# Optimization experiments

Measured on AMD Instinct MI355X. Metric: run time of the kernel, lower is better.

## Reference

```python
import jax, jax.numpy as jnp
import numpy as np

T = 4096          # tokens (batch*seq)
DIM = 2048        # model dim
INTER = 1024      # moe_inter_dim
E = 32            # n_routed_experts
TOPK = 6          # n_activated_experts
G = 8             # n_expert_groups
TOPK_G = 4        # n_limited_groups
SHARED_INTER = 2 * INTER  # n_shared_experts * moe_inter_dim
ROUTE_SCALE = 1.0


def setup_inputs() -> dict:
    key = jax.random.key(0)
    ks = jax.random.split(key, 8)
    s = 0.02
    return {
        "x": jax.random.normal(ks[0], (T, DIM), jnp.float32),
        "gate_w": jax.random.normal(ks[1], (E, DIM), jnp.float32) * s,
        "wg": jax.random.normal(ks[2], (E, DIM, INTER), jnp.float32) * s,   # gate_proj (stored [in,out])
        "wu": jax.random.normal(ks[3], (E, DIM, INTER), jnp.float32) * s,   # up_proj
        "wd": jax.random.normal(ks[4], (E, INTER, DIM), jnp.float32) * s,   # down_proj
        "swg": jax.random.normal(ks[5], (DIM, SHARED_INTER), jnp.float32) * s,
        "swu": jax.random.normal(ks[6], (DIM, SHARED_INTER), jnp.float32) * s,
        "swd": jax.random.normal(ks[7], (SHARED_INTER, DIM), jnp.float32) * s,
    }


def _gate(x, gate_w):
    # scores = softmax(x @ W^T); bias is None since dim != 7168 -> group score = amax
    scores = jax.nn.softmax(x @ gate_w.T, axis=-1)          # [T, E]
    orig = scores
    gs = scores.reshape(x.shape[0], G, E // G)              # [T, G, E/G]
    group_scores = gs.max(axis=-1)                          # [T, G]
    _, gidx = jax.lax.top_k(group_scores, TOPK_G)           # [T, TOPK_G]
    gmask = jnp.zeros((x.shape[0], G), bool).at[
        jnp.arange(x.shape[0])[:, None], gidx].set(True)
    masked = jnp.where(gmask[:, :, None], gs, -jnp.inf).reshape(x.shape[0], E)
    _, idx = jax.lax.top_k(masked, TOPK)                    # [T, TOPK]
    w = jnp.take_along_axis(orig, idx, axis=1) * ROUTE_SCALE  # softmax path: no renorm
    return w, idx


def reference(x, gate_w, wg, wu, wd, swg, swu, swd):
    weights, indices = _gate(x, gate_w)
    # combine[t, e] = routing weight of expert e for token t (0 if not selected)
    combine = (jax.nn.one_hot(indices, E, dtype=x.dtype) * weights[..., None]).sum(axis=1)  # [T, E]
    y = jnp.zeros_like(x)
    for e in range(E):  # fixed small loop over structurally distinct expert params
        h = jax.nn.silu(x @ wg[e]) * (x @ wu[e])            # [T, INTER]
        y = y + (h @ wd[e]) * combine[:, e:e + 1]
    shared = (jax.nn.silu(x @ swg) * (x @ swu)) @ swd       # shared experts MLP
    return y + shared
```

## Files before the change

### kernel.cpp

```cpp
#include <hip/hip_runtime.h>
#include <hip/hip_bf16.h>

typedef float f32x4 __attribute__((ext_vector_type(4)));
typedef __bf16 bf16x8 __attribute__((ext_vector_type(8)));
typedef unsigned short u16;

#define T_TOK 4096
#define DIMK 2048
#define INTERN 1024
#define NEXP 32
#define NTOPK 6
#define NGRP 8
#define NTOPG 4
#define SINTER 2048
#define MAXPADROWS 29184

__device__ __forceinline__ void glds16(const void* g, void* l) {
    auto* gp = (const __attribute__((address_space(1))) int*)(g);
    auto* lp = (__attribute__((address_space(3))) int*)(l);
    __builtin_amdgcn_global_load_lds(gp, lp, 16, 0, 0);
}

__device__ __forceinline__ size_t toff(int row, int k, int K) {
    int g = (k >> 3) & 7;
    return (size_t)(row >> 7) * (size_t)(128 * K) + (size_t)(k >> 6) * 8192 +
           (size_t)((row & 127) * 64 + ((g ^ (row & 7)) << 3) + (k & 7));
}

template <bool CAT>
__device__ __forceinline__ void tile_trans_512(const float* __restrict__ src, int JD, int k0, int j0,
                                               u16* __restrict__ ob, int KOUT, int s, float* tile) {
    const int tid = threadIdx.x;
    {
        const int r = tid >> 3, c8 = (tid & 7) * 8;
        float4 v0 = *reinterpret_cast<const float4*>(&src[(size_t)(k0 + r) * JD + j0 + c8]);
        float4 v1 = *reinterpret_cast<const float4*>(&src[(size_t)(k0 + r) * JD + j0 + c8 + 4]);
        float* tp = &tile[r * 65 + c8];
        tp[0] = v0.x; tp[1] = v0.y; tp[2] = v0.z; tp[3] = v0.w;
        tp[4] = v1.x; tp[5] = v1.y; tp[6] = v1.z; tp[7] = v1.w;
    }
    __syncthreads();
    {
        const int jl = tid >> 3, kh = (tid & 7) * 8;
        const int j = j0 + jl;
        const int n = CAT ? (((j >> 4) << 5) + s * 16 + (j & 15)) : j;
        bf16x8 o;
#pragma unroll
        for (int jj = 0; jj < 8; ++jj) o[jj] = (__bf16)tile[(kh + jj) * 65 + jl];
        *reinterpret_cast<bf16x8*>(ob + toff(n, k0 + kh, KOUT)) = o;
    }
}

__device__ __forceinline__ void gate_wave(const float* __restrict__ x, const float* __restrict__ gw, int t,
                                          int* __restrict__ counts, int* __restrict__ ids,
                                          int* __restrict__ tok2row, float* __restrict__ wtok,
                                          float* __restrict__ logits) {
    const int lane = threadIdx.x & 63;
    const float4* xr = reinterpret_cast<const float4*>(x + (size_t)t * DIMK);
    for (int e = 0; e < NEXP; ++e) {
        const float4* gr = reinterpret_cast<const float4*>(gw + (size_t)e * DIMK);
        float acc = 0.f;
#pragma unroll
        for (int i = 0; i < DIMK / 4 / 64; ++i) {
            float4 xv = xr[lane + i * 64];
            float4 gv = gr[lane + i * 64];
            acc += xv.x * gv.x + xv.y * gv.y + xv.z * gv.z + xv.w * gv.w;
        }
#pragma unroll
        for (int s = 32; s; s >>= 1) acc += __shfl_xor(acc, s);
        if (lane == 0) logits[e] = acc;
    }
    if (lane != 0) return;
    float sc[NEXP];
#pragma unroll
    for (int e = 0; e < NEXP; ++e) sc[e] = logits[e];
    float mx = sc[0];
#pragma unroll
    for (int e = 1; e < NEXP; ++e) mx = fmaxf(mx, sc[e]);
    float ssum = 0.f;
#pragma unroll
    for (int e = 0; e < NEXP; ++e) { sc[e] = __expf(sc[e] - mx); ssum += sc[e]; }
    const float inv = 1.f / ssum;
    float gsc[NGRP];
#pragma unroll
    for (int g = 0; g < NGRP; ++g) {
        float m2 = sc[g * 4];
#pragma unroll
        for (int j = 1; j < 4; ++j) m2 = fmaxf(m2, sc[g * 4 + j]);
        gsc[g] = m2;
    }
    int gsel = 0;
    for (int r = 0; r < NTOPG; ++r) {
        float bv = -1.f; int bi = 0;
#pragma unroll
        for (int g = 0; g < NGRP; ++g) {
            bool c = (((gsel >> g) & 1) == 0) && (gsc[g] > bv);
            bv = c ? gsc[g] : bv; bi = c ? g : bi;
        }
        gsel |= (1 << bi);
    }
    float msk[NEXP];
#pragma unroll
    for (int e = 0; e < NEXP; ++e) msk[e] = ((gsel >> (e >> 2)) & 1) ? sc[e] : -1.f;
    for (int r = 0; r < NTOPK; ++r) {
        float bv = -3.f; int bi = 0;
#pragma unroll
        for (int e = 0; e < NEXP; ++e) {
            bool c = msk[e] > bv;
            bv = c ? msk[e] : bv; bi = c ? e : bi;
        }
#pragma unroll
        for (int e = 0; e < NEXP; ++e) if (e == bi) msk[e] = -2.f;
        float w = bv * inv;
        int slot = atomicAdd(&counts[bi], 1);
        ids[bi * T_TOK + slot] = t;
        tok2row[t * NTOPK + r] = (bi << 12) | slot;
        wtok[t * NTOPK + r] = w;
    }
}

__global__ __launch_bounds__(512) void prep_kernel(
    const float* __restrict__ x, const float* __restrict__ gate_w,
    const float* __restrict__ swg, const float* __restrict__ swu, const float* __restrict__ swd,
    const float* __restrict__ wg, const float* __restrict__ wu,
    u16* __restrict__ xbT, u16* __restrict__ WcatS, u16* __restrict__ swdT, u16* __restrict__ WcatE,
    int* __restrict__ counts, int* __restrict__ ids, int* __restrict__ tok2row, float* __restrict__ wtok) {
    __shared__ float tile[64 * 65];
    int lin = blockIdx.x;
    if (lin < 512) {
        int w = threadIdx.x >> 6;
        gate_wave(x, gate_w, lin * 8 + w, counts, ids, tok2row, wtok, &tile[w * 33]);
    } else if (lin < 2560) {
        int gi = ((lin - 512) * 512 + threadIdx.x) * 8;
        int row = gi >> 11, k = gi & 2047;
        const float4* p = reinterpret_cast<const float4*>(x + gi);
        float4 a = p[0], b = p[1];
        bf16x8 v;
        v[0] = (__bf16)a.x; v[1] = (__bf16)a.y; v[2] = (__bf16)a.z; v[3] = (__bf16)a.w;
        v[4] = (__bf16)b.x; v[5] = (__bf16)b.y; v[6] = (__bf16)b.z; v[7] = (__bf16)b.w;
        *reinterpret_cast<bf16x8*>(xbT + toff(row, k, DIMK)) = v;
    } else if (lin < 4608) {
        int v = lin - 2560;
        int s = v >> 10, u = v & 1023;
        int kt = (u >> 5) & 31, jt = u & 31;
        tile_trans_512<true>((s ? swu : swg), SINTER, kt * 64, jt * 64, WcatS, DIMK, s, tile);
    } else if (lin < 5632) {
        int v = lin - 4608;
        int kt = v >> 5, jt = v & 31;
        tile_trans_512<false>(swd, DIMK, kt * 64, jt * 64, swdT, SINTER, 0, tile);
    } else {
        int u = lin - 5632;
        int e = u >> 10, v = u & 1023;
        int s = (v >> 9) & 1, kt = (v >> 4) & 31, jt = v & 15;
        const float* src = (s ? wu : wg) + (size_t)e * DIMK * INTERN;
        u16* ob = WcatE + (size_t)e * 2048 * DIMK;
        tile_trans_512<true>(src, INTERN, kt * 64, jt * 64, ob, DIMK, s, tile);
    }
}

__global__ void scan_kernel(const int* __restrict__ counts, int* __restrict__ poff) {
    if (threadIdx.x == 0) {
        int o = 0;
        for (int e = 0; e < NEXP; ++e) { poff[e] = o; o += (counts[e] + 127) & ~127; }
    }
}

__device__ __forceinline__ void dev_gemm1(u16* smem, const u16* __restrict__ xbT, const u16* __restrict__ b0,
                                          u16* __restrict__ ho, int bm, int bn, int M, int Mpad, int hbase,
                                          int HKdim, bool gath, int e, const int* __restrict__ ids) {
    u16* Alds = smem;
    u16* Blds = smem + 32768;
    constexpr int NT = DIMK / 64;
    const int tid = threadIdx.x;
    const int t8 = tid * 8;
    size_t aSrc[2][2];
#pragma unroll
    for (int h = 0; h < 2; ++h)
#pragma unroll
        for (int j = 0; j < 2; ++j) {
            int drow = j * 64 + (tid >> 3);
            int row = bm * 256 + h * 128 + drow;
            int tok;
            if (gath) { int cr = row < M ? row : M - 1; tok = ids[e * T_TOK + cr]; }
            else tok = row;
            int slot = (tid & 7) ^ (drow & 7) ^ (tok & 7);
            aSrc[h][j] = (size_t)(tok >> 7) * (size_t)(128 * 2048) + (size_t)((tok & 127) * 64 + slot * 8);
        }
    const u16* bCh[2] = { b0 + (size_t)(2 * bn + 0) * (128 * 2048), b0 + (size_t)(2 * bn + 1) * (128 * 2048) };

    const int lane = tid & 63, wv = tid >> 6;
    const int wr = wv >> 2, wc = wv & 3;
    const int l15 = lane & 15, lk = lane >> 4;

    f32x4 acc[8][4];
#pragma unroll
    for (int m = 0; m < 8; ++m)
#pragma unroll
        for (int n = 0; n < 4; ++n) acc[m][n] = {0.f, 0.f, 0.f, 0.f};

    auto SA = [&](int kt, int h, int buf) {
        glds16(xbT + aSrc[h][0] + (size_t)kt * 8192, &Alds[buf * 16384 + h * 8192 + t8]);
        glds16(xbT + aSrc[h][1] + (size_t)kt * 8192, &Alds[buf * 16384 + h * 8192 + 4096 + t8]);
    };
    auto SB = [&](int kt, int h, int buf) {
        glds16(bCh[h] + (size_t)kt * 8192 + t8, &Blds[buf * 16384 + h * 8192 + t8]);
        glds16(bCh[h] + (size_t)kt * 8192 + 4096 + t8, &Blds[buf * 16384 + h * 8192 + 4096 + t8]);
    };
    bf16x8 afr[4][2], bfr0[2][2], bfr1[2][2];
    auto DSRA = [&](int buf, int mh) {
#pragma unroll
        for (int mi = 0; mi < 4; ++mi)
#pragma unroll
            for (int ki = 0; ki < 2; ++ki) {
                int rl = wr * 128 + mh * 64 + mi * 16 + l15;
                int g = ki * 4 + lk;
                afr[mi][ki] = *reinterpret_cast<const bf16x8*>(
                    &Alds[buf * 16384 + (rl >> 7) * 8192 + (rl & 127) * 64 + ((g ^ (rl & 7)) << 3)]);
            }
    };
    auto DSRB = [&](int buf, int nh, bf16x8 (&bf)[2][2]) {
#pragma unroll
        for (int nj = 0; nj < 2; ++nj)
#pragma unroll
            for (int ki = 0; ki < 2; ++ki) {
                int rc = wc * 64 + (nh * 2 + nj) * 16 + l15;
                int g = ki * 4 + lk;
                bf[nj][ki] = *reinterpret_cast<const bf16x8*>(
                    &Blds[buf * 16384 + (rc >> 7) * 8192 + (rc & 127) * 64 + ((g ^ (rc & 7)) << 3)]);
            }
    };

    SA(0, 0, 0); SA(0, 1, 0);
    SB(0, 0, 0); SB(0, 1, 0);
    SB(1, 0, 1); SB(1, 1, 1);
    asm volatile("s_waitcnt vmcnt(4)" ::: "memory");
    __builtin_amdgcn_s_barrier();

#pragma unroll 1
    for (int t = 0; t < NT; ++t) {
        const int abuf = t & 1;
        const int bbuf = t % 3;
        const int b3 = (t + 2) % 3;
        DSRA(abuf, 0);
        DSRB(bbuf, 0, bfr0);
        if (t + 1 < NT) { SA(t + 1, 0, abuf ^ 1); SA(t + 1, 1, abuf ^ 1); }
        __builtin_amdgcn_s_barrier();
        __builtin_amdgcn_s_setprio(1);
#pragma unroll
        for (int ki = 0; ki < 2; ++ki)
#pragma unroll
            for (int mi = 0; mi < 4; ++mi)
#pragma unroll
                for (int nj = 0; nj < 2; ++nj)
                    acc[mi][nj] = __builtin_amdgcn_mfma_f32_16x16x32_bf16(afr[mi][ki], bfr0[nj][ki], acc[mi][nj], 0, 0, 0);
        __builtin_amdgcn_s_setprio(0);
        __builtin_amdgcn_s_barrier();
        DSRB(bbuf, 1, bfr1);
        if (t + 2 < NT) SB(t + 2, 0, b3);
        __builtin_amdgcn_s_barrier();
        __builtin_amdgcn_s_setprio(1);
#pragma unroll
        for (int ki = 0; ki < 2; ++ki)
#pragma unroll
            for (int mi = 0; mi < 4; ++mi)
#pragma unroll
                for (int nj = 0; nj < 2; ++nj)
                    acc[mi][2 + nj] = __builtin_amdgcn_mfma_f32_16x16x32_bf16(afr[mi][ki], bfr1[nj][ki], acc[mi][2 + nj], 0, 0, 0);
        __builtin_amdgcn_s_setprio(0);
        __builtin_amdgcn_s_barrier();
        DSRA(abuf, 1);
        if (t + 2 < NT) SB(t + 2, 1, b3);
        __builtin_amdgcn_s_barrier();
        __builtin_amdgcn_s_setprio(1);
#pragma unroll
        for (int ki = 0; ki < 2; ++ki)
#pragma unroll
            for (int mi = 0; mi < 4; ++mi)
#pragma unroll
                for (int nj = 0; nj < 2; ++nj)
                    acc[4 + mi][2 + nj] = __builtin_amdgcn_mfma_f32_16x16x32_bf16(afr[mi][ki], bfr1[nj][ki], acc[4 + mi][2 + nj], 0, 0, 0);
        __builtin_amdgcn_s_setprio(0);
        __builtin_amdgcn_s_barrier();
        __builtin_amdgcn_s_setprio(1);
#pragma unroll
        for (int ki = 0; ki < 2; ++ki)
#pragma unroll
            for (int mi = 0; mi < 4; ++mi)
#pragma unroll
                for (int nj = 0; nj < 2; ++nj)
                    acc[4 + mi][nj] = __builtin_amdgcn_mfma_f32_16x16x32_bf16(afr[mi][ki], bfr0[nj][ki], acc[4 + mi][nj], 0, 0, 0);
        __builtin_amdgcn_s_setprio(0);
        if (t + 2 < NT) { asm volatile("s_waitcnt vmcnt(4)" ::: "memory"); }
        else { asm volatile("s_waitcnt vmcnt(0)" ::: "memory"); }
        __builtin_amdgcn_s_barrier();
    }

#pragma unroll
    for (int mI = 0; mI < 8; ++mI) {
#pragma unroll
        for (int r = 0; r < 4; ++r) {
            int grow = bm * 256 + wr * 128 + mI * 16 + lk * 4 + r;
            if (grow < Mpad) {
#pragma unroll
                for (int nh = 0; nh < 2; ++nh) {
                    float gg = acc[mI][nh * 2 + 0][r];
                    float uu = acc[mI][nh * 2 + 1][r];
                    float h = gg / (1.f + __expf(-gg)) * uu;
                    int n = bn * 256 + wc * 64 + nh * 32 + l15;
                    int jcol = ((n >> 5) << 4) + (n & 15);
                    __bf16 hb = (__bf16)h;
                    ho[toff(hbase + grow, jcol, HKdim)] = __builtin_bit_cast(u16, hb);
                }
            }
        }
    }
}

__device__ __forceinline__ void dev_gemm2(u16* smem, const u16* __restrict__ aBase, const u16* __restrict__ bBase,
                                          u16* __restrict__ yo, int bm, int bn, int M, int rowbase, int AKK, int kt0) {
    u16* Alds = smem;
    u16* Blds = smem + 32768;
    constexpr int NT = 16;
    const u16* aCh[2] = { aBase + (size_t)(2 * bm + 0) * (size_t)(128 * AKK) + (size_t)kt0 * 8192,
                          aBase + (size_t)(2 * bm + 1) * (size_t)(128 * AKK) + (size_t)kt0 * 8192 };
    const u16* bCh[2] = { bBase + (size_t)(2 * bn + 0) * (size_t)(128 * AKK) + (size_t)kt0 * 8192,
                          bBase + (size_t)(2 * bn + 1) * (size_t)(128 * AKK) + (size_t)kt0 * 8192 };
    const int tid = threadIdx.x;
    const int t8 = tid * 8;
    const int lane = tid & 63, wv = tid >> 6;
    const int wr = wv >> 2, wc = wv & 3;
    const int l15 = lane & 15, lk = lane >> 4;

    f32x4 acc[8][4];
#pragma unroll
    for (int m = 0; m < 8; ++m)
#pragma unroll
        for (int n = 0; n < 4; ++n) acc[m][n] = {0.f, 0.f, 0.f, 0.f};

    auto SA = [&](int kt, int h, int buf) {
        glds16(aCh[h] + (size_t)kt * 8192 + t8, &Alds[buf * 16384 + h * 8192 + t8]);
        glds16(aCh[h] + (size_t)kt * 8192 + 4096 + t8, &Alds[buf * 16384 + h * 8192 + 4096 + t8]);
    };
    auto SB = [&](int kt, int h, int buf) {
        glds16(bCh[h] + (size_t)kt * 8192 + t8, &Blds[buf * 16384 + h * 8192 + t8]);
        glds16(bCh[h] + (size_t)kt * 8192 + 4096 + t8, &Blds[buf * 16384 + h * 8192 + 4096 + t8]);
    };
    bf16x8 afr[4][2], bfr0[2][2], bfr1[2][2];
    auto DSRA = [&](int buf, int mh) {
#pragma unroll
        for (int mi = 0; mi < 4; ++mi)
#pragma unroll
            for (int ki = 0; ki < 2; ++ki) {
                int rl = wr * 128 + mh * 64 + mi * 16 + l15;
                int g = ki * 4 + lk;
                afr[mi][ki] = *reinterpret_cast<const bf16x8*>(
                    &Alds[buf * 16384 + (rl >> 7) * 8192 + (rl & 127) * 64 + ((g ^ (rl & 7)) << 3)]);
            }
    };
    auto DSRB = [&](int buf, int nh, bf16x8 (&bf)[2][2]) {
#pragma unroll
        for (int nj = 0; nj < 2; ++nj)
#pragma unroll
            for (int ki = 0; ki < 2; ++ki) {
                int rc = wc * 64 + (nh * 2 + nj) * 16 + l15;
                int g = ki * 4 + lk;
                bf[nj][ki] = *reinterpret_cast<const bf16x8*>(
                    &Blds[buf * 16384 + (rc >> 7) * 8192 + (rc & 127) * 64 + ((g ^ (rc & 7)) << 3)]);
            }
    };

    SA(0, 0, 0); SA(0, 1, 0);
    SB(0, 0, 0); SB(0, 1, 0);
    SB(1, 0, 1); SB(1, 1, 1);
    asm volatile("s_waitcnt vmcnt(4)" ::: "memory");
    __builtin_amdgcn_s_barrier();

#pragma unroll 1
    for (int t = 0; t < NT; ++t) {
        const int abuf = t & 1;
        const int bbuf = t % 3;
        const int b3 = (t + 2) % 3;
        DSRA(abuf, 0);
        DSRB(bbuf, 0, bfr0);
        if (t + 1 < NT) { SA(t + 1, 0, abuf ^ 1); SA(t + 1, 1, abuf ^ 1); }
        __builtin_amdgcn_s_barrier();
        __builtin_amdgcn_s_setprio(1);
#pragma unroll
        for (int ki = 0; ki < 2; ++ki)
#pragma unroll
            for (int mi = 0; mi < 4; ++mi)
#pragma unroll
                for (int nj = 0; nj < 2; ++nj)
                    acc[mi][nj] = __builtin_amdgcn_mfma_f32_16x16x32_bf16(afr[mi][ki], bfr0[nj][ki], acc[mi][nj], 0, 0, 0);
        __builtin_amdgcn_s_setprio(0);
        __builtin_amdgcn_s_barrier();
        DSRB(bbuf, 1, bfr1);
        if (t + 2 < NT) SB(t + 2, 0, b3);
        __builtin_amdgcn_s_barrier();
        __builtin_amdgcn_s_setprio(1);
#pragma unroll
        for (int ki = 0; ki < 2; ++ki)
#pragma unroll
            for (int mi = 0; mi < 4; ++mi)
#pragma unroll
                for (int nj = 0; nj < 2; ++nj)
                    acc[mi][2 + nj] = __builtin_amdgcn_mfma_f32_16x16x32_bf16(afr[mi][ki], bfr1[nj][ki], acc[mi][2 + nj], 0, 0, 0);
        __builtin_amdgcn_s_setprio(0);
        __builtin_amdgcn_s_barrier();
        DSRA(abuf, 1);
        if (t + 2 < NT) SB(t + 2, 1, b3);
        __builtin_amdgcn_s_barrier();
        __builtin_amdgcn_s_setprio(1);
#pragma unroll
        for (int ki = 0; ki < 2; ++ki)
#pragma unroll
            for (int mi = 0; mi < 4; ++mi)
#pragma unroll
                for (int nj = 0; nj < 2; ++nj)
                    acc[4 + mi][2 + nj] = __builtin_amdgcn_mfma_f32_16x16x32_bf16(afr[mi][ki], bfr1[nj][ki], acc[4 + mi][2 + nj], 0, 0, 0);
        __builtin_amdgcn_s_setprio(0);
        __builtin_amdgcn_s_barrier();
        __builtin_amdgcn_s_setprio(1);
#pragma unroll
        for (int ki = 0; ki < 2; ++ki)
#pragma unroll
            for (int mi = 0; mi < 4; ++mi)
#pragma unroll
                for (int nj = 0; nj < 2; ++nj)
                    acc[4 + mi][nj] = __builtin_amdgcn_mfma_f32_16x16x32_bf16(afr[mi][ki], bfr0[nj][ki], acc[4 + mi][nj], 0, 0, 0);
        __builtin_amdgcn_s_setprio(0);
        if (t + 2 < NT) { asm volatile("s_waitcnt vmcnt(4)" ::: "memory"); }
        else { asm volatile("s_waitcnt vmcnt(0)" ::: "memory"); }
        __builtin_amdgcn_s_barrier();
    }

#pragma unroll
    for (int mI = 0; mI < 8; ++mI) {
#pragma unroll
        for (int r = 0; r < 4; ++r) {
            int grow = bm * 256 + wr * 128 + mI * 16 + lk * 4 + r;
            if (grow < M) {
                u16* yr = yo + (size_t)(rowbase + grow) * 2048;
#pragma unroll
                for (int ni = 0; ni < 4; ++ni) {
                    int col = bn * 256 + wc * 64 + ni * 16 + l15;
                    __bf16 yb = (__bf16)acc[mI][ni][r];
                    yr[col] = __builtin_bit_cast(u16, yb);
                }
            }
        }
    }
}

__global__ __launch_bounds__(512, 2) void d2_kernel(const u16* __restrict__ xbT, const u16* __restrict__ WcatE,
                                                    u16* __restrict__ H,
                                                    const u16* __restrict__ WcatS, u16* __restrict__ Hs,
                                                    const float* __restrict__ wd, u16* __restrict__ wdTout,
                                                    const int* __restrict__ counts, const int* __restrict__ poff,
                                                    const int* __restrict__ ids) {
    __shared__ u16 smem[81920];
    int lin = blockIdx.x;
    if (lin < 4352) {
        int t = lin / 17, r = lin % 17;
        if (r == 16) {
            int swz = (t & 7) * 32 + (t >> 3);
            int bm = swz & 15, bn = swz >> 4;
            dev_gemm1(smem, xbT, WcatS, Hs, bm, bn, T_TOK, T_TOK, 0, SINTER, false, 0, nullptr);
        } else {
            int u = t * 16 + r;
            int e = 31 - (((u >> 10) << 3) | (u & 7));
            int j = (u >> 3) & 127;
            int bm = j & 15, bn = j >> 4;
            int M = counts[e];
            if (bm * 256 >= M) return;
            dev_gemm1(smem, xbT, WcatE + (size_t)e * 2048 * DIMK, H,
                      bm, bn, M, (M + 127) & ~127, poff[e], INTERN, true, e, ids);
        }
    } else {
        int u = lin - 4352;
        int e = u >> 9, v = u & 511;
        int kt = v >> 5, jt = v & 31;
        tile_trans_512<false>(wd + (size_t)e * INTERN * DIMK, DIMK, kt * 64, jt * 64,
                              wdTout + (size_t)e * DIMK * INTERN, INTERN, 0, (float*)smem);
    }
}

__global__ __launch_bounds__(512) void wdt_kernel(const float* __restrict__ wd, u16* __restrict__ wdTout) {
    __shared__ float tile[64 * 65];
    int u = blockIdx.x;
    int e = u >> 9, v = u & 511;
    tile_trans_512<false>(wd + (size_t)e * INTERN * DIMK, DIMK, (v >> 5) * 64, (v & 31) * 64,
                          wdTout + (size_t)e * DIMK * INTERN, INTERN, 0, tile);
}

__global__ __launch_bounds__(512, 2) void d3_kernel(const u16* __restrict__ H, const u16* __restrict__ wdTu,
                                                    u16* __restrict__ Ye,
                                                    const u16* __restrict__ Hs, const u16* __restrict__ swdT,
                                                    u16* __restrict__ Yss,
                                                    const int* __restrict__ counts, const int* __restrict__ poff) {
    __shared__ u16 smem[81920];
    int lin = blockIdx.x;
    int t = lin / 17, r = lin % 17;
    if (r == 16) {
        int swz = (t & 7) * 32 + (t >> 3);
        int bm = swz & 15, bn = (swz >> 4) & 7, ks = swz >> 7;
        dev_gemm2(smem, Hs, swdT, Yss, bm, bn, T_TOK, ks * T_TOK, SINTER, ks * 16);
    } else {
        int u = t * 16 + r;
        int e = 31 - (((u >> 10) << 3) | (u & 7));
        int j = (u >> 3) & 127;
        int bm = j & 15, bn = j >> 4;
        int M = counts[e];
        if (bm * 256 >= M) return;
        dev_gemm2(smem, H + (size_t)poff[e] * INTERN, wdTu + (size_t)e * 2048 * INTERN, Ye,
                  bm, bn, M, poff[e], INTERN, 0);
    }
}

__global__ __launch_bounds__(256) void combine_kernel(const u16* __restrict__ Yss, const u16* __restrict__ Ye,
                                                      const int* __restrict__ tok2row, const float* __restrict__ wtok,
                                                      const int* __restrict__ poff, float* __restrict__ out) {
    const int t = blockIdx.x;
    const int c = threadIdx.x * 8;
    bf16x8 v0 = *reinterpret_cast<const bf16x8*>(Yss + (size_t)t * 2048 + c);
    bf16x8 v1 = *reinterpret_cast<const bf16x8*>(Yss + (size_t)(T_TOK + t) * 2048 + c);
    float acc[8];
#pragma unroll
    for (int j = 0; j < 8; ++j) acc[j] = (float)v0[j] + (float)v1[j];
#pragma unroll
    for (int r = 0; r < NTOPK; ++r) {
        int pk = tok2row[t * NTOPK + r];
        int e = pk >> 12, sl = pk & 4095;
        int row = poff[e] + sl;
        float w = wtok[t * NTOPK + r];
        bf16x8 v = *reinterpret_cast<const bf16x8*>(Ye + (size_t)row * 2048 + c);
#pragma unroll
        for (int j = 0; j < 8; ++j) acc[j] += w * (float)v[j];
    }
    float4 o0 = {acc[0], acc[1], acc[2], acc[3]};
    float4 o1 = {acc[4], acc[5], acc[6], acc[7]};
    float4* po = reinterpret_cast<float4*>(out + (size_t)t * 2048 + c);
    po[0] = o0; po[1] = o1;
}

extern "C" void kernel_launch(void* const* d_in, const int* in_sizes, int n_in,
                              void* d_out, int out_size, void* d_ws, size_t ws_size,
                              hipStream_t stream) {
    const float* x = (const float*)d_in[0];
    const float* gate_w = (const float*)d_in[1];
    const float* wg = (const float*)d_in[2];
    const float* wu = (const float*)d_in[3];
    const float* wd = (const float*)d_in[4];
    const float* swg = (const float*)d_in[5];
    const float* swu = (const float*)d_in[6];
    const float* swd = (const float*)d_in[7];
    float* out = (float*)d_out;

    char* ws = (char*)d_ws;
    size_t off = 0;
    auto alloc = [&](size_t bytes) {
        void* p = ws + off;
        off = (off + bytes + 255) & ~(size_t)255;
        return p;
    };
    u16* xbT = (u16*)alloc((size_t)T_TOK * DIMK * 2);
    u16* H = (u16*)alloc((size_t)MAXPADROWS * INTERN * 2);
    u16* Hs = (u16*)alloc((size_t)T_TOK * SINTER * 2);
    u16* Ye = (u16*)alloc((size_t)MAXPADROWS * 2048 * 2);
    u16* Yss = (u16*)alloc((size_t)2 * T_TOK * 2048 * 2);
    int* ids = (int*)alloc((size_t)NEXP * T_TOK * 4);
    int* tok2row = (int*)alloc((size_t)T_TOK * NTOPK * 4);
    float* wtok = (float*)alloc((size_t)T_TOK * NTOPK * 4);
    int* counts = (int*)alloc(NEXP * 4);
    int* poff = (int*)alloc(NEXP * 4);
    u16* WcatS = (u16*)alloc((size_t)(2 * SINTER) * DIMK * 2);
    u16* swdT = (u16*)alloc((size_t)DIMK * SINTER * 2);
    u16* WcatE = (u16*)alloc((size_t)NEXP * (2 * INTERN) * DIMK * 2);
    u16* wdT2 = (u16*)alloc((size_t)NEXP * INTERN * DIMK * 2);
    const bool wdFused = (off <= ws_size);
    u16* wdTuse = wdFused ? wdT2 : WcatE;

    hipMemsetAsync(counts, 0, NEXP * 4, stream);

    prep_kernel<<<38400, 512, 0, stream>>>(x, gate_w, swg, swu, swd, wg, wu,
                                           xbT, WcatS, swdT, WcatE, counts, ids, tok2row, wtok);
    scan_kernel<<<1, 64, 0, stream>>>(counts, poff);

    d2_kernel<<<wdFused ? (4352 + 16384) : 4352, 512, 0, stream>>>(
        xbT, WcatE, H, WcatS, Hs, wd, wdTuse, counts, poff, ids);

    if (!wdFused)
        wdt_kernel<<<16384, 512, 0, stream>>>(wd, wdTuse);

    d3_kernel<<<4352, 512, 0, stream>>>(H, wdTuse, Ye, Hs, swdT, Yss, counts, poff);

    combine_kernel<<<T_TOK, 256, 0, stream>>>(Yss, Ye, tok2row, wtok, poff, out);
}
```

Measured before the change: 912.7 us.

## Interleave weight transpose blocks with GEMM blocks and inline expert offset scan

Removes the single-thread scan kernel launch and instead recomputes each expert's padded row offset inline from the counts array wherever it is needed. The fused d2 grid now interleaves 4 GEMM tiles with 15 wd-transpose tiles per group of 19 blocks, so the memory-bound transposes overlap with compute-bound GEMM work instead of trailing after it. The cost is a small serial loop over up to 32 counts in every block, including each combine thread, plus a few wasted blocks in the padded grid.

```diff
diff --git a/kernel.cpp b/kernel.cpp
--- a/kernel.cpp
+++ b/kernel.cpp
@@ -25,6 +25,12 @@
     int g = (k >> 3) & 7;
     return (size_t)(row >> 7) * (size_t)(128 * K) + (size_t)(k >> 6) * 8192 +
            (size_t)((row & 127) * 64 + ((g ^ (row & 7)) << 3) + (k & 7));
+}
+
+__device__ __forceinline__ int poff_of(const int* __restrict__ counts, int e) {
+    int o = 0;
+    for (int i = 0; i < e; ++i) o += (counts[i] + 127) & ~127;
+    return o;
 }
 
 template <bool CAT>
@@ -158,13 +164,6 @@
     }
 }
 
-__global__ void scan_kernel(const int* __restrict__ counts, int* __restrict__ poff) {
-    if (threadIdx.x == 0) {
-        int o = 0;
-        for (int e = 0; e < NEXP; ++e) { poff[e] = o; o += (counts[e] + 127) & ~127; }
-    }
-}
-
 __device__ __forceinline__ void dev_gemm1(u16* smem, const u16* __restrict__ xbT, const u16* __restrict__ b0,
                                           u16* __restrict__ ho, int bm, int bn, int M, int Mpad, int hbase,
                                           int HKdim, bool gath, int e, const int* __restrict__ ids) {
@@ -456,12 +455,20 @@
                                                     u16* __restrict__ H,
                                                     const u16* __restrict__ WcatS, u16* __restrict__ Hs,
                                                     const float* __restrict__ wd, u16* __restrict__ wdTout,
-                                                    const int* __restrict__ counts, const int* __restrict__ poff,
-                                                    const int* __restrict__ ids) {
+                                                    const int* __restrict__ counts,
+                                                    const int* __restrict__ ids, int interleaved) {
     __shared__ u16 smem[81920];
     int lin = blockIdx.x;
-    if (lin < 4352) {
-        int t = lin / 17, r = lin % 17;
+    int core = -1, trans = -1;
+    if (interleaved) {
+        int unit = lin / 19, sl = lin % 19;
+        if (sl < 4) { int c = unit * 4 + sl; if (c < 4352) core = c; }
+        else { int u = unit * 15 + (sl - 4); if (u < 16384) trans = u; }
+    } else {
+        core = lin;
+    }
+    if (core >= 0) {
+        int t = core / 17, r = core % 17;
         if (r == 16) {
             int swz = (t & 7) * 32 + (t >> 3);
             int bm = swz & 15, bn = swz >> 4;
@@ -474,11 +481,10 @@
             int M = counts[e];
             if (bm * 256 >= M) return;
             dev_gemm1(smem, xbT, WcatE + (size_t)e * 2048 * DIMK, H,
-                      bm, bn, M, (M + 127) & ~127, poff[e], INTERN, true, e, ids);
+                      bm, bn, M, (M + 127) & ~127, poff_of(counts, e), INTERN, true, e, ids);
         }
-    } else {
-        int u = lin - 4352;
-        int e = u >> 9, v = u & 511;
+    } else if (trans >= 0) {
+        int e = trans >> 9, v = trans & 511;
         int kt = v >> 5, jt = v & 31;
         tile_trans_512<false>(wd + (size_t)e * INTERN * DIMK, DIMK, kt * 64, jt * 64,
                               wdTout + (size_t)e * DIMK * INTERN, INTERN, 0, (float*)smem);
@@ -497,7 +503,7 @@
                                                     u16* __restrict__ Ye,
                                                     const u16* __restrict__ Hs, const u16* __restrict__ swdT,
                                                     u16* __restrict__ Yss,
-                                                    const int* __restrict__ counts, const int* __restrict__ poff) {
+                                                    const int* __restrict__ counts) {
     __shared__ u16 smem[81920];
     int lin = blockIdx.x;
     int t = lin / 17, r = lin % 17;
@@ -512,14 +518,15 @@
         int bm = j & 15, bn = j >> 4;
         int M = counts[e];
         if (bm * 256 >= M) return;
-        dev_gemm2(smem, H + (size_t)poff[e] * INTERN, wdTu + (size_t)e * 2048 * INTERN, Ye,
-                  bm, bn, M, poff[e], INTERN, 0);
+        int pe = poff_of(counts, e);
+        dev_gemm2(smem, H + (size_t)pe * INTERN, wdTu + (size_t)e * 2048 * INTERN, Ye,
+                  bm, bn, M, pe, INTERN, 0);
     }
 }
 
 __global__ __launch_bounds__(256) void combine_kernel(const u16* __restrict__ Yss, const u16* __restrict__ Ye,
                                                       const int* __restrict__ tok2row, const float* __restrict__ wtok,
-                                                      const int* __restrict__ poff, float* __restrict__ out) {
+                                                      const int* __restrict__ counts, float* __restrict__ out) {
     const int t = blockIdx.x;
     const int c = threadIdx.x * 8;
     bf16x8 v0 = *reinterpret_cast<const bf16x8*>(Yss + (size_t)t * 2048 + c);
@@ -531,7 +538,7 @@
     for (int r = 0; r < NTOPK; ++r) {
         int pk = tok2row[t * NTOPK + r];
         int e = pk >> 12, sl = pk & 4095;
-        int row = poff[e] + sl;
+        int row = poff_of(counts, e) + sl;
         float w = wtok[t * NTOPK + r];
         bf16x8 v = *reinterpret_cast<const bf16x8*>(Ye + (size_t)row * 2048 + c);
 #pragma unroll
@@ -572,7 +579,6 @@
     int* tok2row = (int*)alloc((size_t)T_TOK * NTOPK * 4);
     float* wtok = (float*)alloc((size_t)T_TOK * NTOPK * 4);
     int* counts = (int*)alloc(NEXP * 4);
-    int* poff = (int*)alloc(NEXP * 4);
     u16* WcatS = (u16*)alloc((size_t)(2 * SINTER) * DIMK * 2);
     u16* swdT = (u16*)alloc((size_t)DIMK * SINTER * 2);
     u16* WcatE = (u16*)alloc((size_t)NEXP * (2 * INTERN) * DIMK * 2);
@@ -584,15 +590,14 @@
 
     prep_kernel<<<38400, 512, 0, stream>>>(x, gate_w, swg, swu, swd, wg, wu,
                                            xbT, WcatS, swdT, WcatE, counts, ids, tok2row, wtok);
-    scan_kernel<<<1, 64, 0, stream>>>(counts, poff);
-
-    d2_kernel<<<wdFused ? (4352 + 16384) : 4352, 512, 0, stream>>>(
-        xbT, WcatE, H, WcatS, Hs, wd, wdTuse, counts, poff, ids);
+
+    d2_kernel<<<wdFused ? 20767 : 4352, 512, 0, stream>>>(
+        xbT, WcatE, H, WcatS, Hs, wd, wdTuse, counts, ids, wdFused ? 1 : 0);
 
     if (!wdFused)
         wdt_kernel<<<16384, 512, 0, stream>>>(wd, wdTuse);
 
-    d3_kernel<<<4352, 512, 0, stream>>>(H, wdTuse, Ye, Hs, swdT, Yss, counts, poff);
-
-    combine_kernel<<<T_TOK, 256, 0, stream>>>(Yss, Ye, tok2row, wtok, poff, out);
-}
+    d3_kernel<<<4352, 512, 0, stream>>>(H, wdTuse, Ye, Hs, swdT, Yss, counts);
+
+    combine_kernel<<<T_TOK, 256, 0, stream>>>(Yss, Ye, tok2row, wtok, counts, out);
+}
```

Result: slower. 1.053 ms (+15.3%).
